# Kernel tuning notes

Measured on AMD Instinct MI355X. Metric: run time of the kernel, lower is better.

## Reference

```python
import jax, jax.numpy as jnp
import numpy as np

N_NODES = 1000
HIDDEN = 256
IN_DIM = 128
N_EDGES = 64000


def setup_inputs() -> dict:
    key = jax.random.key(0)
    ks = jax.random.split(key, 24)
    inp = {
        "x": jax.random.normal(ks[0], (N_NODES, IN_DIM), dtype=jnp.float32),
        "edge_index": jax.random.randint(ks[1], (2, N_EDGES), 0, N_NODES, dtype=jnp.int64),
    }
    dims = [(HIDDEN, 2 * IN_DIM)] + [(HIDDEN, 2 * HIDDEN)] * 4
    for l, (dout, din) in enumerate(dims):
        s0 = 1.0 / np.sqrt(din)
        s1 = 1.0 / np.sqrt(HIDDEN)
        inp[f"w{l}_0"] = jax.random.normal(ks[2 + 4 * l], (dout, din), dtype=jnp.float32) * s0
        inp[f"b{l}_0"] = jax.random.normal(ks[3 + 4 * l], (dout,), dtype=jnp.float32) * s0
        inp[f"w{l}_1"] = jax.random.normal(ks[4 + 4 * l], (HIDDEN, HIDDEN), dtype=jnp.float32) * s1
        inp[f"b{l}_1"] = jax.random.normal(ks[5 + 4 * l], (HIDDEN,), dtype=jnp.float32) * s1
    return inp


def _edge_conv(x, src, dst, w1, b1, w2, b2):
    # gather endpoint features per edge: [E, D]
    x_i = x[dst]  # destination (edge_index[1])
    x_j = x[src]  # source (edge_index[0])
    m = jnp.concatenate([x_i, x_j - x_i], axis=-1)  # [E, 2D]
    h = jax.nn.relu(m @ w1.T + b1) @ w2.T + b2      # 2-layer MLP, [E, HIDDEN]
    # scatter-max to destination nodes (include_self=False -> empty rows = 0)
    agg = jax.ops.segment_max(h, dst, num_segments=N_NODES)
    agg = jnp.where(jnp.isneginf(agg), jnp.zeros((), agg.dtype), agg)
    return jax.nn.relu(agg)


def reference(x, edge_index, w0_0, b0_0, w0_1, b0_1, w1_0, b1_0, w1_1, b1_1,
              w2_0, b2_0, w2_1, b2_1, w3_0, b3_0, w3_1, b3_1, w4_0, b4_0, w4_1, b4_1):
    src = edge_index[0]
    dst = edge_index[1]
    params = [(w0_0, b0_0, w0_1, b0_1), (w1_0, b1_0, w1_1, b1_1),
              (w2_0, b2_0, w2_1, b2_1), (w3_0, b3_0, w3_1, b3_1),
              (w4_0, b4_0, w4_1, b4_1)]
    h = x
    for (w1, b1, w2, b2) in params:
        h = _edge_conv(h, src, dst, w1, b1, w2, b2)
    return h
```

## Files before the change

kernel.cpp:

```cpp
#include <hip/hip_runtime.h>

#define NN 1000
#define NE 64000
#define HH 256

typedef _Float16 half8 __attribute__((ext_vector_type(8)));
typedef float floatx4 __attribute__((ext_vector_type(4)));

struct PrepArgs { const float* w0[5]; const float* w1[5]; };

__global__ __launch_bounds__(256) void k_prep(PrepArgs pa,
                                              _Float16* wnode, _Float16* w2h,
                                              int* counts, float* aggA) {
    int gtid = blockIdx.x * 256 + threadIdx.x;
    int gstride = gridDim.x * 256;
    for (int i = gtid; i < 1024; i += gstride) counts[i] = 0;
    for (int l = 0; l < 5; l++) {
        const int KK = l ? 8 : 4;
        const int D = KK * 32;
        const int lgKK = l ? 3 : 2;
        const float* w0 = pa.w0[l];
        _Float16* wn = wnode + l * 131072;
        for (int i = gtid; i < 16384 * KK; i += gstride) {
            int j = i & 7;
            int lane = (i >> 3) & 63;
            int nt = (i >> 9) & 1;
            int kk = (i >> 10) & (KK - 1);
            int slice = i >> (10 + lgKK);
            int mn = lane & 15, q = lane >> 4;
            int n = slice * 32 + nt * 16 + mn;
            int k = kk * 32 + q * 8 + j;
            float v = (n < 256) ? (w0[n * 2 * D + k] - w0[n * 2 * D + D + k])
                                : w0[(n - 256) * 2 * D + D + k];
            wn[i] = (_Float16)v;
        }
        const float* w1 = pa.w1[l];
        _Float16* w2 = w2h + l * 65536;
        for (int i = gtid; i < 65536; i += gstride) {
            int j = i & 7;
            int lane = (i >> 3) & 63;
            int nt = (i >> 9) & 3;
            int kk = (i >> 11) & 7;
            int ws = (i >> 14) & 3;
            int mn = lane & 15, q = lane >> 4;
            int row = ws * 64 + nt * 16 + mn;
            int col = kk * 32 + q * 8 + j;
            w2[i] = (_Float16)w1[row * 256 + col];
        }
    }
    floatx4 z = {0.f, 0.f, 0.f, 0.f};
    floatx4* p4 = (floatx4*)aggA;
    for (int i = gtid; i < NN * HH / 4; i += gstride) p4[i] = z;
}

template <int NK>
__device__ inline void node_tile(const float* __restrict__ X,
                                 const _Float16* __restrict__ Wn, const float* __restrict__ b0,
                                 _Float16* __restrict__ out, int bid) {
    const int Kd = NK * 32;
    int t = threadIdx.x;
    int wave = t >> 6, lane = t & 63;
    int q = lane >> 4, mn = lane & 15;
    int m0 = (bid % 63) * 16;
    int n0 = (bid / 63) * 128 + wave * 32;
    int slice = (bid / 63) * 4 + wave;
    int rr = m0 + mn;
    if (rr >= NN) rr = NN - 1;

    half8 afa[NK];
    half8 bfa[NK][2];
#pragma unroll
    for (int kk = 0; kk < NK; kk++) {
        int ka = kk * 32 + q * 8;
        const float* p = X + (size_t)rr * Kd + ka;
        floatx4 x0 = *(const floatx4*)p;
        floatx4 x1 = *(const floatx4*)(p + 4);
        half8 aa;
#pragma unroll
        for (int j = 0; j < 4; j++) { aa[j] = (_Float16)x0[j]; aa[4 + j] = (_Float16)x1[j]; }
        afa[kk] = aa;
        bfa[kk][0] = *(const half8*)(Wn + (((slice * NK + kk) * 2 + 0) * 64 + lane) * 8);
        bfa[kk][1] = *(const half8*)(Wn + (((slice * NK + kk) * 2 + 1) * 64 + lane) * 8);
    }
    floatx4 acc[2] = {};
#pragma unroll
    for (int kk = 0; kk < NK; kk++) {
        acc[0] = __builtin_amdgcn_mfma_f32_16x16x32_f16(afa[kk], bfa[kk][0], acc[0], 0, 0, 0);
        acc[1] = __builtin_amdgcn_mfma_f32_16x16x32_f16(afa[kk], bfa[kk][1], acc[1], 0, 0, 0);
    }
#pragma unroll
    for (int nt = 0; nt < 2; nt++) {
        int col = n0 + nt * 16 + mn;
        float bias = (col < 256) ? b0[col] : 0.f;
#pragma unroll
        for (int r2 = 0; r2 < 4; r2++) {
            int orow = m0 + q * 4 + r2;
            if (orow < NN)
                out[(size_t)orow * 512 + col] = (_Float16)(acc[nt][r2] + bias);
        }
    }
}

__global__ __launch_bounds__(256) void k_hist_node0(const int* __restrict__ ei,
                                                    int* __restrict__ counts,
                                                    const float* __restrict__ X,
                                                    const _Float16* __restrict__ Wn,
                                                    const float* __restrict__ b0,
                                                    _Float16* __restrict__ out) {
    int bid = blockIdx.x;
    if (bid < 4) {
        for (int e = bid * 256 + threadIdx.x; e < NE; e += 4 * 256)
            atomicAdd(&counts[ei[NE + e] & 1023], 1);
    } else {
        node_tile<4>(X, Wn, b0, out, bid - 4);
    }
}

__global__ __launch_bounds__(256) void k_scan(const int* __restrict__ counts,
                                              int* __restrict__ cursor) {
    __shared__ int s[256];
    int t = threadIdx.x;
    int base = t * 4;
    int c4[4]; int sum = 0;
#pragma unroll
    for (int j = 0; j < 4; j++) { c4[j] = counts[base + j]; sum += c4[j]; }
    s[t] = sum;
    __syncthreads();
    for (int d = 1; d < 256; d <<= 1) {
        int v = (t >= d) ? s[t - d] : 0;
        __syncthreads();
        s[t] += v;
        __syncthreads();
    }
    int run = (t > 0) ? s[t - 1] : 0;
#pragma unroll
    for (int j = 0; j < 4; j++) { cursor[base + j] = run; run += c4[j]; }
}

__global__ __launch_bounds__(256) void k_scatter(const int* __restrict__ ei,
                                                 int* __restrict__ cursor,
                                                 int* __restrict__ ssrc, int* __restrict__ sdst) {
    int e = blockIdx.x * blockDim.x + threadIdx.x;
    if (e < NE) {
        int s = ei[e] & 1023, d = ei[NE + e] & 1023;
        int pos = atomicAdd(&cursor[d], 1);
        if (pos < NE) {
            ssrc[pos] = s;
            sdst[pos] = d;
        }
    }
}

__global__ __launch_bounds__(256) void k_node_zero(const float* __restrict__ agg_in,
                                                   const _Float16* __restrict__ Wn,
                                                   const float* __restrict__ b0,
                                                   _Float16* __restrict__ out,
                                                   float* __restrict__ agg_next) {
    int bid = blockIdx.x;
    if (bid < 252) {
        node_tile<8>(agg_in, Wn, b0, out, bid);
    } else {
        floatx4 z = {0.f, 0.f, 0.f, 0.f};
        floatx4* p4 = (floatx4*)agg_next;
        for (int i = (bid - 252) * 256 + (int)threadIdx.x; i < NN * HH / 4; i += 64 * 256)
            p4[i] = z;
    }
}

__global__ __launch_bounds__(256, 4) void edge_gemm(const _Float16* __restrict__ node_ab,
                          const int* __restrict__ ssrc, const int* __restrict__ sdst,
                          const _Float16* __restrict__ W2, const float* __restrict__ b2,
                          float* __restrict__ agg) {
    __shared__ _Float16 h1[64 * 256];
    __shared__ int sd[64];
    int t = threadIdx.x;
    int e0 = blockIdx.x * 64;
    int wave = t >> 6, lane = t & 63;
    int q = lane >> 4, mn = lane & 15;
    int n0 = wave * 64;
    const _Float16* W2w = W2 + wave * 16384;

    if (t < 64) sd[t] = sdst[e0 + t];
    {
        int row = t & 63;
        int cb = (t >> 6) * 8;
        int dn = sdst[e0 + row], sn = ssrc[e0 + row];
        const _Float16* pa = node_ab + (size_t)dn * 512 + cb * 8;
        const _Float16* pb = node_ab + (size_t)sn * 512 + 256 + cb * 8;
        half8 av[8], bv[8];
#pragma unroll
        for (int i = 0; i < 8; i++) av[i] = *(const half8*)(pa + i * 8);
#pragma unroll
        for (int i = 0; i < 8; i++) bv[i] = *(const half8*)(pb + i * 8);
#pragma unroll
        for (int i = 0; i < 8; i++) {
            int c = cb + i;
            int p = (c & ~7) | ((c ^ row) & 7);
            half8 hv = av[i] + bv[i];
#pragma unroll
            for (int j = 0; j < 8; j++) hv[j] = hv[j] > (_Float16)0 ? hv[j] : (_Float16)0;
            *(half8*)(&h1[row * 256 + p * 8]) = hv;
        }
    }
    __syncthreads();

    floatx4 acc[4][4] = {};
#pragma unroll
    for (int kk = 0; kk < 8; kk++) {
        half8 bf[4];
#pragma unroll
        for (int nt = 0; nt < 4; nt++)
            bf[nt] = *(const half8*)(W2w + (kk * 4 + nt) * 512 + lane * 8);
        half8 af[4];
#pragma unroll
        for (int mt = 0; mt < 4; mt++) {
            int r = mt * 16 + mn;
            int c = kk * 4 + q;
            int p = (c & ~7) | ((c ^ r) & 7);
            af[mt] = *(const half8*)(&h1[r * 256 + p * 8]);
        }
#pragma unroll
        for (int mt = 0; mt < 4; mt++)
#pragma unroll
            for (int nt = 0; nt < 4; nt++)
                acc[mt][nt] = __builtin_amdgcn_mfma_f32_16x16x32_f16(af[mt], bf[nt], acc[mt][nt], 0, 0, 0);
    }

#pragma unroll
    for (int nt = 0; nt < 4; nt++) {
        int col = n0 + nt * 16 + mn;
        float bias = b2[col];
        int curd = -1;
        float curv = 0.f;
#pragma unroll
        for (int mt = 0; mt < 4; mt++) {
#pragma unroll
            for (int r2 = 0; r2 < 4; r2++) {
                int er = mt * 16 + q * 4 + r2;
                int d = sd[er];
                float v = acc[mt][nt][r2] + bias;
                v = v > 0.f ? v : 0.f;
                if (d != curd) {
                    if (curd >= 0 && curv > 0.f)
                        atomicMax((unsigned int*)(agg + (size_t)curd * HH + col), __float_as_uint(curv));
                    curd = d;
                    curv = v;
                } else {
                    curv = fmaxf(curv, v);
                }
            }
        }
        if (curd >= 0 && curv > 0.f)
            atomicMax((unsigned int*)(agg + (size_t)curd * HH + col), __float_as_uint(curv));
    }
}

extern "C" void kernel_launch(void* const* d_in, const int* in_sizes, int n_in,
                              void* d_out, int out_size, void* d_ws, size_t ws_size,
                              hipStream_t stream) {
    const float* x = (const float*)d_in[0];
    const int* ei = (const int*)d_in[1];
    PrepArgs pa;
    const float* b0s[5];
    const float* b1s[5];
    for (int l = 0; l < 5; l++) {
        pa.w0[l] = (const float*)d_in[2 + 4 * l];
        b0s[l] = (const float*)d_in[3 + 4 * l];
        pa.w1[l] = (const float*)d_in[4 + 4 * l];
        b1s[l] = (const float*)d_in[5 + 4 * l];
    }

    int* ssrc = (int*)d_ws;
    int* sdst = ssrc + NE;
    int* counts = sdst + NE;
    int* cursor = counts + 1024;
    _Float16* node_ab = (_Float16*)(cursor + 1024);
    float* aggA = (float*)(node_ab + 1024 * 512);
    float* aggB = aggA + NN * HH;
    _Float16* wnode = (_Float16*)(aggB + NN * HH);
    _Float16* w2h = wnode + 5 * 131072;

    hipLaunchKernelGGL(k_prep, dim3(256), dim3(256), 0, stream, pa, wnode, w2h, counts, aggA);
    hipLaunchKernelGGL(k_hist_node0, dim3(256), dim3(256), 0, stream, ei, counts, x, wnode, b0s[0], node_ab);
    hipLaunchKernelGGL(k_scan, dim3(1), dim3(256), 0, stream, counts, cursor);
    hipLaunchKernelGGL(k_scatter, dim3((NE + 255) / 256), dim3(256), 0, stream, ei, cursor, ssrc, sdst);

    float* aggs[5] = {aggA, aggB, aggA, aggB, (float*)d_out};
    for (int l = 0; l < 5; l++) {
        hipLaunchKernelGGL(edge_gemm, dim3(NE / 64), dim3(256), 0, stream,
                           node_ab, ssrc, sdst, w2h + (size_t)l * 65536, b1s[l], aggs[l]);
        if (l < 4)
            hipLaunchKernelGGL(k_node_zero, dim3(252 + 64), dim3(256), 0, stream,
                               aggs[l], wnode + (size_t)(l + 1) * 131072, b0s[l + 1],
                               node_ab, aggs[l + 1]);
    }
}
```

Measured before the change: 292.5 us.

## Double-buffer edge tiles in edge_gemm to overlap gathers with MFMA

Each edge_gemm block now handles two 64-edge tiles, keeping two LDS buffers. It issues the gathers for the second tile's node features before running the MFMA and atomic-max epilogue on the first, hiding gather latency behind compute. The cost is a doubled LDS footprint of about 64KB, a lower launch-bounds occupancy hint of 2, and half as many blocks (500), which may reduce latency hiding across waves.

```diff
diff --git a/kernel.cpp b/kernel.cpp
--- a/kernel.cpp
+++ b/kernel.cpp
@@ -167,27 +167,31 @@
     }
 }
 
-__global__ __launch_bounds__(256, 4) void edge_gemm(const _Float16* __restrict__ node_ab,
+__global__ __launch_bounds__(256, 2) void edge_gemm(const _Float16* __restrict__ node_ab,
                           const int* __restrict__ ssrc, const int* __restrict__ sdst,
                           const _Float16* __restrict__ W2, const float* __restrict__ b2,
                           float* __restrict__ agg) {
-    __shared__ _Float16 h1[64 * 256];
-    __shared__ int sd[64];
+    __shared__ _Float16 h1[2][64 * 256];
+    __shared__ int sd[2][64];
     int t = threadIdx.x;
-    int e0 = blockIdx.x * 64;
     int wave = t >> 6, lane = t & 63;
     int q = lane >> 4, mn = lane & 15;
     int n0 = wave * 64;
+    int row = t & 63, cb = (t >> 6) * 8;
     const _Float16* W2w = W2 + wave * 16384;
 
-    if (t < 64) sd[t] = sdst[e0 + t];
+    float bias[4];
+#pragma unroll
+    for (int nt = 0; nt < 4; nt++) bias[nt] = b2[n0 + nt * 16 + mn];
+
+    int tile0 = blockIdx.x * 2;
+    half8 av[8], bv[8];
     {
-        int row = t & 63;
-        int cb = (t >> 6) * 8;
+        int e0 = tile0 * 64;
+        if (t < 64) sd[0][t] = sdst[e0 + t];
         int dn = sdst[e0 + row], sn = ssrc[e0 + row];
         const _Float16* pa = node_ab + (size_t)dn * 512 + cb * 8;
         const _Float16* pb = node_ab + (size_t)sn * 512 + 256 + cb * 8;
-        half8 av[8], bv[8];
 #pragma unroll
         for (int i = 0; i < 8; i++) av[i] = *(const half8*)(pa + i * 8);
 #pragma unroll
@@ -199,59 +203,87 @@
             half8 hv = av[i] + bv[i];
 #pragma unroll
             for (int j = 0; j < 8; j++) hv[j] = hv[j] > (_Float16)0 ? hv[j] : (_Float16)0;
-            *(half8*)(&h1[row * 256 + p * 8]) = hv;
+            *(half8*)(&h1[0][row * 256 + p * 8]) = hv;
         }
     }
     __syncthreads();
 
-    floatx4 acc[4][4] = {};
-#pragma unroll
-    for (int kk = 0; kk < 8; kk++) {
-        half8 bf[4];
-#pragma unroll
-        for (int nt = 0; nt < 4; nt++)
-            bf[nt] = *(const half8*)(W2w + (kk * 4 + nt) * 512 + lane * 8);
-        half8 af[4];
-#pragma unroll
-        for (int mt = 0; mt < 4; mt++) {
-            int r = mt * 16 + mn;
-            int c = kk * 4 + q;
-            int p = (c & ~7) | ((c ^ r) & 7);
-            af[mt] = *(const half8*)(&h1[r * 256 + p * 8]);
-        }
-#pragma unroll
-        for (int mt = 0; mt < 4; mt++)
+#pragma unroll
+    for (int it = 0; it < 2; it++) {
+        const int cur = it & 1, nxt = cur ^ 1;
+        if (it + 1 < 2) {
+            int e1 = (tile0 + it + 1) * 64;
+            if (t < 64) sd[nxt][t] = sdst[e1 + t];
+            int dn = sdst[e1 + row], sn = ssrc[e1 + row];
+            const _Float16* pa = node_ab + (size_t)dn * 512 + cb * 8;
+            const _Float16* pb = node_ab + (size_t)sn * 512 + 256 + cb * 8;
+#pragma unroll
+            for (int i = 0; i < 8; i++) av[i] = *(const half8*)(pa + i * 8);
+#pragma unroll
+            for (int i = 0; i < 8; i++) bv[i] = *(const half8*)(pb + i * 8);
+        }
+
+        floatx4 acc[4][4] = {};
+#pragma unroll
+        for (int kk = 0; kk < 8; kk++) {
+            half8 bf[4];
 #pragma unroll
             for (int nt = 0; nt < 4; nt++)
-                acc[mt][nt] = __builtin_amdgcn_mfma_f32_16x16x32_f16(af[mt], bf[nt], acc[mt][nt], 0, 0, 0);
-    }
-
-#pragma unroll
-    for (int nt = 0; nt < 4; nt++) {
-        int col = n0 + nt * 16 + mn;
-        float bias = b2[col];
-        int curd = -1;
-        float curv = 0.f;
-#pragma unroll
-        for (int mt = 0; mt < 4; mt++) {
-#pragma unroll
-            for (int r2 = 0; r2 < 4; r2++) {
-                int er = mt * 16 + q * 4 + r2;
-                int d = sd[er];
-                float v = acc[mt][nt][r2] + bias;
-                v = v > 0.f ? v : 0.f;
-                if (d != curd) {
-                    if (curd >= 0 && curv > 0.f)
-                        atomicMax((unsigned int*)(agg + (size_t)curd * HH + col), __float_as_uint(curv));
-                    curd = d;
-                    curv = v;
-                } else {
-                    curv = fmaxf(curv, v);
+                bf[nt] = *(const half8*)(W2w + (kk * 4 + nt) * 512 + lane * 8);
+            half8 af[4];
+#pragma unroll
+            for (int mt = 0; mt < 4; mt++) {
+                int r = mt * 16 + mn;
+                int c = kk * 4 + q;
+                int p = (c & ~7) | ((c ^ r) & 7);
+                af[mt] = *(const half8*)(&h1[cur][r * 256 + p * 8]);
+            }
+#pragma unroll
+            for (int mt = 0; mt < 4; mt++)
+#pragma unroll
+                for (int nt = 0; nt < 4; nt++)
+                    acc[mt][nt] = __builtin_amdgcn_mfma_f32_16x16x32_f16(af[mt], bf[nt], acc[mt][nt], 0, 0, 0);
+        }
+
+#pragma unroll
+        for (int nt = 0; nt < 4; nt++) {
+            int col = n0 + nt * 16 + mn;
+            int curd = -1;
+            float curv = 0.f;
+#pragma unroll
+            for (int mt = 0; mt < 4; mt++) {
+#pragma unroll
+                for (int r2 = 0; r2 < 4; r2++) {
+                    int er = mt * 16 + q * 4 + r2;
+                    int d = sd[cur][er];
+                    float v = acc[mt][nt][r2] + bias[nt];
+                    v = v > 0.f ? v : 0.f;
+                    if (d != curd) {
+                        if (curd >= 0 && curv > 0.f)
+                            atomicMax((unsigned int*)(agg + (size_t)curd * HH + col), __float_as_uint(curv));
+                        curd = d;
+                        curv = v;
+                    } else {
+                        curv = fmaxf(curv, v);
+                    }
                 }
             }
-        }
-        if (curd >= 0 && curv > 0.f)
-            atomicMax((unsigned int*)(agg + (size_t)curd * HH + col), __float_as_uint(curv));
+            if (curd >= 0 && curv > 0.f)
+                atomicMax((unsigned int*)(agg + (size_t)curd * HH + col), __float_as_uint(curv));
+        }
+
+        if (it + 1 < 2) {
+#pragma unroll
+            for (int i = 0; i < 8; i++) {
+                int c = cb + i;
+                int p = (c & ~7) | ((c ^ row) & 7);
+                half8 hv = av[i] + bv[i];
+#pragma unroll
+                for (int j = 0; j < 8; j++) hv[j] = hv[j] > (_Float16)0 ? hv[j] : (_Float16)0;
+                *(half8*)(&h1[nxt][row * 256 + p * 8]) = hv;
+            }
+            __syncthreads();
+        }
     }
 }
 
@@ -287,7 +319,7 @@
 
     float* aggs[5] = {aggA, aggB, aggA, aggB, (float*)d_out};
     for (int l = 0; l < 5; l++) {
-        hipLaunchKernelGGL(edge_gemm, dim3(NE / 64), dim3(256), 0, stream,
+        hipLaunchKernelGGL(edge_gemm, dim3(NE / 128), dim3(256), 0, stream,
                            node_ab, ssrc, sdst, w2h + (size_t)l * 65536, b1s[l], aggs[l]);
         if (l < 4)
             hipLaunchKernelGGL(k_node_zero, dim3(252 + 64), dim3(256), 0, stream,
```

Result: no change. 295.7 us (+1.1%).

## Replace edge-tiled atomic scatter-max with per-destination segmented reduction

Applied to the files above, without the earlier changes.

The edge MLP kernel now launches one block per pair of destination nodes. Each block walks that pair's CSR edge segment in 64-edge chunks, keeps the running max in registers, and writes the final result with plain stores. This removes the global atomicMax traffic and the separate zeroing passes over the aggregation buffers, so the zeroing work is dropped from k_prep and the node kernel. The cost is load imbalance, since segments vary in length and partial 64-edge chunks waste MFMA work. There is also a lower grid count (500 blocks) with an occupancy hint of 2.

```diff
diff --git a/kernel.cpp b/kernel.cpp
--- a/kernel.cpp
+++ b/kernel.cpp
@@ -3,6 +3,8 @@
 #define NN 1000
 #define NE 64000
 #define HH 256
+#define NG 2
+#define NB (NN / NG)
 
 typedef _Float16 half8 __attribute__((ext_vector_type(8)));
 typedef float floatx4 __attribute__((ext_vector_type(4)));
@@ -11,7 +13,7 @@
 
 __global__ __launch_bounds__(256) void k_prep(PrepArgs pa,
                                               _Float16* wnode, _Float16* w2h,
-                                              int* counts, float* aggA) {
+                                              int* counts) {
     int gtid = blockIdx.x * 256 + threadIdx.x;
     int gstride = gridDim.x * 256;
     for (int i = gtid; i < 1024; i += gstride) counts[i] = 0;
@@ -48,9 +50,6 @@
             w2[i] = (_Float16)w1[row * 256 + col];
         }
     }
-    floatx4 z = {0.f, 0.f, 0.f, 0.f};
-    floatx4* p4 = (floatx4*)aggA;
-    for (int i = gtid; i < NN * HH / 4; i += gstride) p4[i] = z;
 }
 
 template <int NK>
@@ -151,107 +150,116 @@
     }
 }
 
-__global__ __launch_bounds__(256) void k_node_zero(const float* __restrict__ agg_in,
-                                                   const _Float16* __restrict__ Wn,
-                                                   const float* __restrict__ b0,
-                                                   _Float16* __restrict__ out,
-                                                   float* __restrict__ agg_next) {
-    int bid = blockIdx.x;
-    if (bid < 252) {
-        node_tile<8>(agg_in, Wn, b0, out, bid);
-    } else {
-        floatx4 z = {0.f, 0.f, 0.f, 0.f};
-        floatx4* p4 = (floatx4*)agg_next;
-        for (int i = (bid - 252) * 256 + (int)threadIdx.x; i < NN * HH / 4; i += 64 * 256)
-            p4[i] = z;
-    }
-}
-
-__global__ __launch_bounds__(256, 4) void edge_gemm(const _Float16* __restrict__ node_ab,
+__global__ __launch_bounds__(256) void k_node(const float* __restrict__ agg_in,
+                                              const _Float16* __restrict__ Wn,
+                                              const float* __restrict__ b0,
+                                              _Float16* __restrict__ out) {
+    node_tile<8>(agg_in, Wn, b0, out, blockIdx.x);
+}
+
+__global__ __launch_bounds__(256, 2) void edge_seg(const _Float16* __restrict__ node_ab,
                           const int* __restrict__ ssrc, const int* __restrict__ sdst,
+                          const int* __restrict__ cursor,
                           const _Float16* __restrict__ W2, const float* __restrict__ b2,
                           float* __restrict__ agg) {
     __shared__ _Float16 h1[64 * 256];
     __shared__ int sd[64];
     int t = threadIdx.x;
-    int e0 = blockIdx.x * 64;
     int wave = t >> 6, lane = t & 63;
     int q = lane >> 4, mn = lane & 15;
     int n0 = wave * 64;
+    int row = t & 63, cb = (t >> 6) * 8;
     const _Float16* W2w = W2 + wave * 16384;
 
-    if (t < 64) sd[t] = sdst[e0 + t];
-    {
-        int row = t & 63;
-        int cb = (t >> 6) * 8;
-        int dn = sdst[e0 + row], sn = ssrc[e0 + row];
-        const _Float16* pa = node_ab + (size_t)dn * 512 + cb * 8;
-        const _Float16* pb = node_ab + (size_t)sn * 512 + 256 + cb * 8;
-        half8 av[8], bv[8];
-#pragma unroll
-        for (int i = 0; i < 8; i++) av[i] = *(const half8*)(pa + i * 8);
-#pragma unroll
-        for (int i = 0; i < 8; i++) bv[i] = *(const half8*)(pb + i * 8);
-#pragma unroll
-        for (int i = 0; i < 8; i++) {
-            int c = cb + i;
-            int p = (c & ~7) | ((c ^ row) & 7);
-            half8 hv = av[i] + bv[i];
-#pragma unroll
-            for (int j = 0; j < 8; j++) hv[j] = hv[j] > (_Float16)0 ? hv[j] : (_Float16)0;
-            *(half8*)(&h1[row * 256 + p * 8]) = hv;
-        }
-    }
-    __syncthreads();
-
-    floatx4 acc[4][4] = {};
-#pragma unroll
-    for (int kk = 0; kk < 8; kk++) {
-        half8 bf[4];
-#pragma unroll
-        for (int nt = 0; nt < 4; nt++)
-            bf[nt] = *(const half8*)(W2w + (kk * 4 + nt) * 512 + lane * 8);
-        half8 af[4];
+    int nd0 = blockIdx.x * NG;
+    int e_start = nd0 ? cursor[nd0 - 1] : 0;
+    int e_end = cursor[nd0 + NG - 1];
+
+    float bias[4];
+#pragma unroll
+    for (int nt = 0; nt < 4; nt++) bias[nt] = b2[n0 + nt * 16 + mn];
+
+    float vmax[NG][4];
+#pragma unroll
+    for (int g = 0; g < NG; g++)
+#pragma unroll
+        for (int nt = 0; nt < 4; nt++) vmax[g][nt] = 0.f;
+
+    for (int e0 = e_start; e0 < e_end; e0 += 64) {
+        if (t < 64) sd[t] = (e0 + t < e_end) ? (sdst[e0 + t] - nd0) : -1;
+        {
+            int e = e0 + row;
+            if (e >= e_end) e = e_end - 1;
+            int dn = sdst[e], sn = ssrc[e];
+            const _Float16* pa = node_ab + (size_t)dn * 512 + cb * 8;
+            const _Float16* pb = node_ab + (size_t)sn * 512 + 256 + cb * 8;
+            half8 av[8], bv[8];
+#pragma unroll
+            for (int i = 0; i < 8; i++) av[i] = *(const half8*)(pa + i * 8);
+#pragma unroll
+            for (int i = 0; i < 8; i++) bv[i] = *(const half8*)(pb + i * 8);
+#pragma unroll
+            for (int i = 0; i < 8; i++) {
+                int c = cb + i;
+                int p = (c & ~7) | ((c ^ row) & 7);
+                half8 hv = av[i] + bv[i];
+#pragma unroll
+                for (int j = 0; j < 8; j++) hv[j] = hv[j] > (_Float16)0 ? hv[j] : (_Float16)0;
+                *(half8*)(&h1[row * 256 + p * 8]) = hv;
+            }
+        }
+        __syncthreads();
+
+        floatx4 acc[4][4] = {};
+#pragma unroll
+        for (int kk = 0; kk < 8; kk++) {
+            half8 bf[4];
+#pragma unroll
+            for (int nt = 0; nt < 4; nt++)
+                bf[nt] = *(const half8*)(W2w + (kk * 4 + nt) * 512 + lane * 8);
+            half8 af[4];
+#pragma unroll
+            for (int mt = 0; mt < 4; mt++) {
+                int r = mt * 16 + mn;
+                int c = kk * 4 + q;
+                int p = (c & ~7) | ((c ^ r) & 7);
+                af[mt] = *(const half8*)(&h1[r * 256 + p * 8]);
+            }
+#pragma unroll
+            for (int mt = 0; mt < 4; mt++)
+#pragma unroll
+                for (int nt = 0; nt < 4; nt++)
+                    acc[mt][nt] = __builtin_amdgcn_mfma_f32_16x16x32_f16(af[mt], bf[nt], acc[mt][nt], 0, 0, 0);
+        }
+
 #pragma unroll
         for (int mt = 0; mt < 4; mt++) {
-            int r = mt * 16 + mn;
-            int c = kk * 4 + q;
-            int p = (c & ~7) | ((c ^ r) & 7);
-            af[mt] = *(const half8*)(&h1[r * 256 + p * 8]);
-        }
-#pragma unroll
-        for (int mt = 0; mt < 4; mt++)
-#pragma unroll
-            for (int nt = 0; nt < 4; nt++)
-                acc[mt][nt] = __builtin_amdgcn_mfma_f32_16x16x32_f16(af[mt], bf[nt], acc[mt][nt], 0, 0, 0);
-    }
-
-#pragma unroll
-    for (int nt = 0; nt < 4; nt++) {
-        int col = n0 + nt * 16 + mn;
-        float bias = b2[col];
-        int curd = -1;
-        float curv = 0.f;
-#pragma unroll
-        for (int mt = 0; mt < 4; mt++) {
 #pragma unroll
             for (int r2 = 0; r2 < 4; r2++) {
-                int er = mt * 16 + q * 4 + r2;
-                int d = sd[er];
-                float v = acc[mt][nt][r2] + bias;
-                v = v > 0.f ? v : 0.f;
-                if (d != curd) {
-                    if (curd >= 0 && curv > 0.f)
-                        atomicMax((unsigned int*)(agg + (size_t)curd * HH + col), __float_as_uint(curv));
-                    curd = d;
-                    curv = v;
-                } else {
-                    curv = fmaxf(curv, v);
+                int dl = sd[mt * 16 + q * 4 + r2];
+                if (dl >= 0) {
+#pragma unroll
+                    for (int nt = 0; nt < 4; nt++) {
+                        float v = acc[mt][nt][r2] + bias[nt];
+                        v = v > 0.f ? v : 0.f;
+                        vmax[dl][nt] = fmaxf(vmax[dl][nt], v);
+                    }
                 }
             }
         }
-        if (curd >= 0 && curv > 0.f)
-            atomicMax((unsigned int*)(agg + (size_t)curd * HH + col), __float_as_uint(curv));
+        __syncthreads();
+    }
+
+#pragma unroll
+    for (int g = 0; g < NG; g++) {
+#pragma unroll
+        for (int nt = 0; nt < 4; nt++) {
+            float v = vmax[g][nt];
+            v = fmaxf(v, __shfl_xor(v, 16, 64));
+            v = fmaxf(v, __shfl_xor(v, 32, 64));
+            if (q == 0)
+                agg[(size_t)(nd0 + g) * HH + n0 + nt * 16 + mn] = v;
+        }
     }
 }
 
@@ -280,18 +288,17 @@
     _Float16* wnode = (_Float16*)(aggB + NN * HH);
     _Float16* w2h = wnode + 5 * 131072;
 
-    hipLaunchKernelGGL(k_prep, dim3(256), dim3(256), 0, stream, pa, wnode, w2h, counts, aggA);
+    hipLaunchKernelGGL(k_prep, dim3(256), dim3(256), 0, stream, pa, wnode, w2h, counts);
     hipLaunchKernelGGL(k_hist_node0, dim3(256), dim3(256), 0, stream, ei, counts, x, wnode, b0s[0], node_ab);
     hipLaunchKernelGGL(k_scan, dim3(1), dim3(256), 0, stream, counts, cursor);
     hipLaunchKernelGGL(k_scatter, dim3((NE + 255) / 256), dim3(256), 0, stream, ei, cursor, ssrc, sdst);
 
     float* aggs[5] = {aggA, aggB, aggA, aggB, (float*)d_out};
     for (int l = 0; l < 5; l++) {
-        hipLaunchKernelGGL(edge_gemm, dim3(NE / 64), dim3(256), 0, stream,
-                           node_ab, ssrc, sdst, w2h + (size_t)l * 65536, b1s[l], aggs[l]);
+        hipLaunchKernelGGL(edge_seg, dim3(NB), dim3(256), 0, stream,
+                           node_ab, ssrc, sdst, cursor, w2h + (size_t)l * 65536, b1s[l], aggs[l]);
         if (l < 4)
-            hipLaunchKernelGGL(k_node_zero, dim3(252 + 64), dim3(256), 0, stream,
-                               aggs[l], wnode + (size_t)(l + 1) * 131072, b0s[l + 1],
-                               node_ab, aggs[l + 1]);
-    }
-}
+            hipLaunchKernelGGL(k_node, dim3(252), dim3(256), 0, stream,
+                               aggs[l], wnode + (size_t)(l + 1) * 131072, b0s[l + 1], node_ab);
+    }
+}
```

Result: slower. 330.9 us (+13.1%).
